# Performance work log

Measured on AMD Instinct MI355X. Metric: run time of the kernel, lower is better.

The kernel has to match this reference:

```python
import jax, jax.numpy as jnp
import numpy as np

NEIGHBOR_NUM = 4
POOLING_RATE = 4


def setup_inputs() -> dict:
    key = jax.random.key(0)
    k1, k2, k3 = jax.random.split(key, 3)
    B, N, C = 4, 8192, 256
    vertices = jax.random.normal(k1, (B, N, 3), dtype=jnp.float32)
    feature_map = jax.random.normal(k2, (B, N, C), dtype=jnp.float32)
    pool_num = N // POOLING_RATE
    sample_idx = jax.random.permutation(k3, N)[:pool_num].astype(jnp.int32)  # torch.randperm(N)[:pool_num]
    return {"vertices": vertices, "feature_map": feature_map, "radius": 1, "sample_idx": sample_idx}


def _query_ball_point(radius, nsample, xyz):
    # xyz: [B, N, 3]; self-query (new_xyz == xyz)
    B, N, _ = xyz.shape
    sq = jnp.sum(xyz * xyz, axis=-1)                       # [B, N]
    dist = -2.0 * jnp.einsum('bnc,bmc->bnm', xyz, xyz)     # [B, N, N]
    dist = dist + sq[:, :, None] + sq[:, None, :]
    # original code zeroes the diagonal (self-distance)
    diag = jnp.arange(N)
    dist = dist.at[:, diag, diag].set(0.0)
    # mark out-of-ball entries with sentinel N, sort indices, keep first nsample
    idx = jnp.arange(N, dtype=jnp.int32)
    group_idx = jnp.where(dist > radius ** 2, jnp.int32(N), idx[None, None, :])  # [B, N, N]
    group_idx = jnp.sort(group_idx, axis=-1)[:, :, :nsample]                     # [B, N, nsample]
    group_first = group_idx[:, :, :1]
    group_idx = jnp.where(group_idx == N, group_first, group_idx)
    return group_idx


def reference(vertices, feature_map, radius, sample_idx):
    B, N, _ = vertices.shape
    neighbor_index = _query_ball_point(radius, NEIGHBOR_NUM, vertices)          # [B, N, k]
    bidx = jnp.arange(B)[:, None, None]
    neighbor_feature = feature_map[bidx, neighbor_index]                        # [B, N, k, C]
    pooled_feature = jnp.max(neighbor_feature, axis=2)                          # [B, N, C]
    vertices_pool = vertices[:, sample_idx, :]                                  # [B, pool, 3]
    feature_map_pool = pooled_feature[:, sample_idx, :]                         # [B, pool, C]
    return (vertices_pool, feature_map_pool)
```

## Files before the change

kernel.cpp:

```cpp
#include <hip/hip_runtime.h>


#define BB 4
#define NN 8192
#define CC 256
#define PP 2048
#define KK 4
#define CH 8

__global__ __launch_bounds__(256) void pool_layer_kernel(
    const float* __restrict__ vertices,
    const float* __restrict__ feat,
    const int*   __restrict__ radius_p,
    const int*   __restrict__ sample_idx,
    float* __restrict__ out_v,
    float* __restrict__ out_f)
{
    const int wave = threadIdx.x >> 6;
    const int lane = threadIdx.x & 63;
    const int q    = blockIdx.x * 4 + wave;
    const int b    = q >> 11;
    const int i    = q & (PP - 1);
    const int n    = sample_idx[i];

    const float* vb = vertices + (size_t)b * NN * 3;

    const float xn0 = vb[n * 3 + 0];
    const float xn1 = vb[n * 3 + 1];
    const float xn2 = vb[n * 3 + 2];
    const float sqn = __fadd_rn(__fadd_rn(__fmul_rn(xn0, xn0),
                                          __fmul_rn(xn1, xn1)),
                                __fmul_rn(xn2, xn2));

    const int   r  = radius_p[0];
    const float r2 = (float)(r * r);

    if (lane < 3) {
        out_v[((size_t)b * PP + i) * 3 + lane] = vb[n * 3 + lane];
    }

    int cand[KK];
    int cnt = 0;
    for (int base = 0; base < NN && cnt < KK; base += 64 * CH) {
        unsigned long long masks[CH];
        #pragma unroll
        for (int c = 0; c < CH; ++c) {
            const int m = base + 64 * c + lane;
            const float x0 = vb[m * 3 + 0];
            const float x1 = vb[m * 3 + 1];
            const float x2 = vb[m * 3 + 2];
            const float sqm = __fadd_rn(__fadd_rn(__fmul_rn(x0, x0),
                                                  __fmul_rn(x1, x1)),
                                        __fmul_rn(x2, x2));
            const float dot = __fadd_rn(__fadd_rn(__fmul_rn(xn0, x0),
                                                  __fmul_rn(xn1, x1)),
                                        __fmul_rn(xn2, x2));
            const float dist = __fadd_rn(__fadd_rn(__fmul_rn(-2.0f, dot), sqn), sqm);
            masks[c] = __ballot((m == n) || !(dist > r2));
        }
        #pragma unroll
        for (int c = 0; c < CH; ++c) {
            unsigned long long mask = masks[c];
            while (mask && cnt < KK) {
                const int l = __ffsll(mask) - 1;
                cand[cnt++] = base + 64 * c + l;
                mask &= (mask - 1);
            }
        }
    }
    for (int j = cnt; j < KK; ++j) cand[j] = cand[0];

    const float4* f0 = (const float4*)(feat + ((size_t)b * NN + cand[0]) * CC);
    const float4* f1 = (const float4*)(feat + ((size_t)b * NN + cand[1]) * CC);
    const float4* f2 = (const float4*)(feat + ((size_t)b * NN + cand[2]) * CC);
    const float4* f3 = (const float4*)(feat + ((size_t)b * NN + cand[3]) * CC);
    const float4 a0 = f0[lane];
    const float4 a1 = f1[lane];
    const float4 a2 = f2[lane];
    const float4 a3 = f3[lane];
    float4 o;
    o.x = fmaxf(fmaxf(a0.x, a1.x), fmaxf(a2.x, a3.x));
    o.y = fmaxf(fmaxf(a0.y, a1.y), fmaxf(a2.y, a3.y));
    o.z = fmaxf(fmaxf(a0.z, a1.z), fmaxf(a2.z, a3.z));
    o.w = fmaxf(fmaxf(a0.w, a1.w), fmaxf(a2.w, a3.w));
    ((float4*)(out_f + ((size_t)b * PP + i) * CC))[lane] = o;
}

extern "C" void kernel_launch(void* const* d_in, const int* in_sizes, int n_in,
                              void* d_out, int out_size, void* d_ws, size_t ws_size,
                              hipStream_t stream) {
    const float* vertices   = (const float*)d_in[0];
    const float* feat       = (const float*)d_in[1];
    const int*   radius_p   = (const int*)d_in[2];
    const int*   sample_idx = (const int*)d_in[3];

    float* out_v = (float*)d_out;
    float* out_f = out_v + (size_t)BB * PP * 3;

    const int queries = BB * PP;
    dim3 grid(queries / 4), block(256);
    pool_layer_kernel<<<grid, block, 0, stream>>>(
        vertices, feat, radius_p, sample_idx, out_v, out_f);
}
```

Measured before the change: 95.31 us.

## Double-buffer vertex batch loads in registers and enlarge scan chunk

The ball-query scan now prefetches the next batch of candidate vertex coordinates into registers while computing distances on the current batch, and the batch width doubles from 8 to 16 chunks of 64. The aim is to hide global load latency behind the distance and ballot work. In exchange it uses more registers, which can lower occupancy, and it wastes a prefetch on early exit since most queries find their neighbors in the first batch.

```diff
diff --git a/kernel.cpp b/kernel.cpp
--- a/kernel.cpp
+++ b/kernel.cpp
@@ -6,7 +6,9 @@
 #define CC 256
 #define PP 2048
 #define KK 4
-#define CH 8
+#define CH 16
+#define BATCH (64 * CH)
+#define NBATCH (NN / BATCH)
 
 __global__ __launch_bounds__(256) void pool_layer_kernel(
     const float* __restrict__ vertices,
@@ -21,17 +23,24 @@
     const int q    = blockIdx.x * 4 + wave;
     const int b    = q >> 11;
     const int i    = q & (PP - 1);
-    const int n    = sample_idx[i];
-
     const float* vb = vertices + (size_t)b * NN * 3;
 
+    float px[CH], py[CH], pz[CH];
+    #pragma unroll
+    for (int c = 0; c < CH; ++c) {
+        const int m = c * 64 + lane;
+        px[c] = vb[m * 3 + 0];
+        py[c] = vb[m * 3 + 1];
+        pz[c] = vb[m * 3 + 2];
+    }
+
+    const int n = sample_idx[i];
     const float xn0 = vb[n * 3 + 0];
     const float xn1 = vb[n * 3 + 1];
     const float xn2 = vb[n * 3 + 2];
     const float sqn = __fadd_rn(__fadd_rn(__fmul_rn(xn0, xn0),
                                           __fmul_rn(xn1, xn1)),
                                 __fmul_rn(xn2, xn2));
-
     const int   r  = radius_p[0];
     const float r2 = (float)(r * r);
 
@@ -41,14 +50,23 @@
 
     int cand[KK];
     int cnt = 0;
-    for (int base = 0; base < NN && cnt < KK; base += 64 * CH) {
+    for (int bat = 0; bat < NBATCH && cnt < KK; ++bat) {
+        const int nb = (bat + 1 < NBATCH) ? (bat + 1) : bat;
+        float nx[CH], ny[CH], nz[CH];
+        #pragma unroll
+        for (int c = 0; c < CH; ++c) {
+            const int m = nb * BATCH + c * 64 + lane;
+            nx[c] = vb[m * 3 + 0];
+            ny[c] = vb[m * 3 + 1];
+            nz[c] = vb[m * 3 + 2];
+        }
+
+        const int base = bat * BATCH;
         unsigned long long masks[CH];
         #pragma unroll
         for (int c = 0; c < CH; ++c) {
-            const int m = base + 64 * c + lane;
-            const float x0 = vb[m * 3 + 0];
-            const float x1 = vb[m * 3 + 1];
-            const float x2 = vb[m * 3 + 2];
+            const int m = base + c * 64 + lane;
+            const float x0 = px[c], x1 = py[c], x2 = pz[c];
             const float sqm = __fadd_rn(__fadd_rn(__fmul_rn(x0, x0),
                                                   __fmul_rn(x1, x1)),
                                         __fmul_rn(x2, x2));
@@ -63,10 +81,13 @@
             unsigned long long mask = masks[c];
             while (mask && cnt < KK) {
                 const int l = __ffsll(mask) - 1;
-                cand[cnt++] = base + 64 * c + l;
+                cand[cnt++] = base + c * 64 + l;
                 mask &= (mask - 1);
             }
         }
+
+        #pragma unroll
+        for (int c = 0; c < CH; ++c) { px[c] = nx[c]; py[c] = ny[c]; pz[c] = nz[c]; }
     }
     for (int j = cnt; j < KK; ++j) cand[j] = cand[0];
 
```

New measurement: 99.39 us. +4.3%, slower.
